# Kernel tuning notes

Measured on AMD Instinct MI355X. Metric: run time of the kernel, lower is better.

## Reference

```python
import jax, jax.numpy as jnp
import numpy as np

N_NODES = 100000
N_EDGES = 300000


def _nnconv(x, src, dst, edge_attr, w, b, root, bias, in_dim, out_dim):
    # PyG NNConv with aggr='add': W_e = nn(edge_attr_e).reshape(in, out)
    # msg_e = x[src_e] @ W_e ; out_i = sum_e->i msg_e + x_i @ root + bias
    W = (edge_attr @ w.T + b).reshape(-1, in_dim, out_dim)        # [E, in, out]
    msg = jnp.einsum('ei,eio->eo', x[src], W)                     # [E, out]
    agg = jax.ops.segment_sum(msg, dst, num_segments=x.shape[0])  # [N, out]
    return agg + x @ root + bias


def setup_inputs() -> dict:
    key = jax.random.key(0)
    ks = jax.random.split(key, 16)
    x = jax.random.normal(ks[0], (N_NODES, 2), dtype=jnp.float32)
    edge_index = jax.random.randint(ks[1], (2, N_EDGES), 0, N_NODES)
    edge_attr = jax.random.uniform(ks[2], (N_EDGES, 2), dtype=jnp.float32)

    def lin(k, out_d, in_d):
        s = 1.0 / np.sqrt(in_d)
        kw, kb = jax.random.split(k)
        w = jax.random.uniform(kw, (out_d, in_d), minval=-s, maxval=s)
        b = jax.random.uniform(kb, (out_d,), minval=-s, maxval=s)
        return w, b

    nn1_w, nn1_b = lin(ks[3], 64, 2)      # edge MLP for conv1: 2 -> 2*32
    nn2_w, nn2_b = lin(ks[4], 1024, 2)    # edge MLP for conv2: 2 -> 32*32
    root1 = jax.random.normal(ks[5], (2, 32)) * (1.0 / np.sqrt(2))
    bias1 = jnp.zeros((32,), dtype=jnp.float32)
    root2 = jax.random.normal(ks[6], (32, 32)) * (1.0 / np.sqrt(32))
    bias2 = jnp.zeros((32,), dtype=jnp.float32)
    fc1_w, fc1_b = lin(ks[7], 32, 32)
    fc2_w, fc2_b = lin(ks[8], 1, 32)
    return {
        'x': x, 'edge_index': edge_index, 'edge_attr': edge_attr,
        'nn1_w': nn1_w, 'nn1_b': nn1_b, 'root1': root1, 'bias1': bias1,
        'nn2_w': nn2_w, 'nn2_b': nn2_b, 'root2': root2, 'bias2': bias2,
        'fc1_w': fc1_w, 'fc1_b': fc1_b, 'fc2_w': fc2_w, 'fc2_b': fc2_b,
    }


def reference(x, edge_index, edge_attr, nn1_w, nn1_b, root1, bias1,
              nn2_w, nn2_b, root2, bias2, fc1_w, fc1_b, fc2_w, fc2_b):
    src, dst = edge_index[0], edge_index[1]
    h = jax.nn.relu(_nnconv(x, src, dst, edge_attr, nn1_w, nn1_b, root1, bias1, 2, 32))
    h = jax.nn.relu(_nnconv(h, src, dst, edge_attr, nn2_w, nn2_b, root2, bias2, 32, 32))
    h = jax.nn.relu(h @ fc1_w.T + fc1_b)
    return h @ fc2_w.T + fc2_b  # [N, 1]
```

## Files before the change

### kernel.cpp

```cpp
#include <hip/hip_runtime.h>

#define N_NODES 100000
#define N_EDGES 300000
#define CAP 32
#define NPAIRS (N_NODES / 2)
#define NT 64
#define NTILES ((N_NODES + NT - 1) / NT)
#define PAD 129

__global__ __launch_bounds__(256) void zero_cnt_kernel(int4* __restrict__ p,
                                                       int n4)
{
    int i = blockIdx.x * 256 + threadIdx.x;
    if (i < n4) p[i] = make_int4(0, 0, 0, 0);
}

__global__ __launch_bounds__(256) void scatter_kernel(
    const int* __restrict__ src, const int* __restrict__ dst,
    const float* __restrict__ ea,
    int* __restrict__ cnt, float4* __restrict__ slots)
{
    int e = blockIdx.x * 256 + threadIdx.x;
    if (e >= N_EDGES) return;
    int s = src[e], d = dst[e];
    float2 a = ((const float2*)ea)[e];
    int pos = atomicAdd(&cnt[d], 1);
    if (pos < CAP)
        slots[(size_t)d * CAP + pos] = make_float4(__int_as_float(s), a.x, a.y, 0.f);
}

__global__ __launch_bounds__(256) void prepack_kernel(
    const float* __restrict__ nn2_w, const float* __restrict__ nn2_b,
    const float* __restrict__ root2, const float* __restrict__ fc1_w,
    float* __restrict__ Wt, float* __restrict__ Ft)
{
    int t = blockIdx.x * 256 + threadIdx.x;
    if (t < 4096) {
        int i = t >> 5, o = t & 31;
        int ii = i & 31;
        float v;
        if (i < 32)      v = nn2_w[(ii * 32 + o) * 2];
        else if (i < 64) v = nn2_w[(ii * 32 + o) * 2 + 1];
        else if (i < 96) v = nn2_b[ii * 32 + o];
        else             v = root2[ii * 32 + o];
        Wt[i * 32 + o] = v;
    }
    if (t < 1024) {
        int o = t >> 5, j = t & 31;
        Ft[o * 32 + j] = fc1_w[j * 32 + o];
    }
}

__global__ __launch_bounds__(256) void layer1a_kernel(
    const float* __restrict__ x, const int* __restrict__ cnt,
    const float4* __restrict__ slots,
    const float* __restrict__ nn1_w, const float* __restrict__ nn1_b,
    const float* __restrict__ root1, const float* __restrict__ bias1,
    float* __restrict__ h1)
{
    int t = threadIdx.x;
    int wv = t >> 6, lane = t & 63, o = lane & 31, hihalf = lane >> 5;
    int pair = blockIdx.x * 4 + wv;
    if (pair >= NPAIRS) return;
    int n = pair * 2 + hihalf;
    int c = min(cnt[n], CAP);
    float u0 = 0.f, u1 = 0.f, u2 = 0.f, u3 = 0.f, u4 = 0.f, u5 = 0.f;
    if (o < c) {
        float4 sl = slots[(size_t)n * CAP + o];
        int s = __float_as_int(sl.x);
        float2 xv = ((const float2*)x)[s];
        u0 = xv.x * sl.y; u1 = xv.x * sl.z;
        u2 = xv.y * sl.y; u3 = xv.y * sl.z;
        u4 = xv.x;        u5 = xv.y;
    }
    #pragma unroll
    for (int m = 1; m < 32; m <<= 1) {
        u0 += __shfl_xor(u0, m, 32);
        u1 += __shfl_xor(u1, m, 32);
        u2 += __shfl_xor(u2, m, 32);
        u3 += __shfl_xor(u3, m, 32);
        u4 += __shfl_xor(u4, m, 32);
        u5 += __shfl_xor(u5, m, 32);
    }
    float2 w0 = ((const float2*)nn1_w)[o];
    float2 w1 = ((const float2*)nn1_w)[32 + o];
    float2 xn = ((const float2*)x)[n];
    float agg = u0 * w0.x + u1 * w0.y + u2 * w1.x + u3 * w1.y
              + u4 * nn1_b[o] + u5 * nn1_b[32 + o];
    float h = agg + fmaf(xn.x, root1[o], fmaf(xn.y, root1[32 + o], bias1[o]));
    h1[(size_t)n * 32 + o] = fmaxf(h, 0.f);
}

__global__ __launch_bounds__(256) void gather_uvw_kernel(
    const float* __restrict__ h1, const int* __restrict__ cnt,
    const float4* __restrict__ slots, float* __restrict__ UVW)
{
    int t = threadIdx.x, o = t & 31;
    int n = blockIdx.x * 8 + (t >> 5);
    if (n >= N_NODES) return;
    int c = min(cnt[n], CAP);
    float U = 0.f, V = 0.f, W = 0.f;
    for (int j0 = 0; j0 < c; j0 += 4) {
        bool g1 = j0 + 1 < c, g2 = j0 + 2 < c, g3 = j0 + 3 < c;
        float4 s0 = slots[(size_t)n * CAP + j0];
        float4 s1 = g1 ? slots[(size_t)n * CAP + j0 + 1] : s0;
        float4 s2 = g2 ? slots[(size_t)n * CAP + j0 + 2] : s0;
        float4 s3 = g3 ? slots[(size_t)n * CAP + j0 + 3] : s0;
        int i0 = __float_as_int(s0.x), i1 = __float_as_int(s1.x);
        int i2 = __float_as_int(s2.x), i3 = __float_as_int(s3.x);
        float v0 = h1[(size_t)i0 * 32 + o];
        float v1 = h1[(size_t)i1 * 32 + o];
        float v2 = h1[(size_t)i2 * 32 + o];
        float v3 = h1[(size_t)i3 * 32 + o];
        U = fmaf(s0.y, v0, U);
        U = fmaf(g1 ? s1.y : 0.f, v1, U);
        U = fmaf(g2 ? s2.y : 0.f, v2, U);
        U = fmaf(g3 ? s3.y : 0.f, v3, U);
        V = fmaf(s0.z, v0, V);
        V = fmaf(g1 ? s1.z : 0.f, v1, V);
        V = fmaf(g2 ? s2.z : 0.f, v2, V);
        V = fmaf(g3 ? s3.z : 0.f, v3, V);
        W += v0;
        W = fmaf(g1 ? 1.f : 0.f, v1, W);
        W = fmaf(g2 ? 1.f : 0.f, v2, W);
        W = fmaf(g3 ? 1.f : 0.f, v3, W);
    }
    size_t b = (size_t)n * 96;
    UVW[b + o]      = U;
    UVW[b + 32 + o] = V;
    UVW[b + 64 + o] = W;
}

__global__ __launch_bounds__(512, 6) void matvec_fc_kernel(
    const float* __restrict__ UVW, const float* __restrict__ h1,
    const float* __restrict__ Wt, const float* __restrict__ Ft,
    const float* __restrict__ bias2,
    const float* __restrict__ fc1_b, const float* __restrict__ fc2_w,
    const float* __restrict__ fc2_b, float* __restrict__ out)
{
    __shared__ float ld[NT][PAD];
    __shared__ float h2s[NT][33];
    float* psf = &ld[0][0];

    int t = threadIdx.x;
    int wv = t >> 6;
    int wvu = __builtin_amdgcn_readfirstlane(wv);
    int lane = t & 63;
    int tb = blockIdx.x * NT;

    {
        const float4* uvw4 = (const float4*)(UVW + (size_t)tb * 96);
        #pragma unroll
        for (int it = 0; it < 3; ++it) {
            int f4i = it * 512 + t;
            float4 v = uvw4[f4i];
            int node = f4i / 24, c4 = (f4i % 24) * 4;
            ld[node][c4]     = v.x;
            ld[node][c4 + 1] = v.y;
            ld[node][c4 + 2] = v.z;
            ld[node][c4 + 3] = v.w;
        }
        const float4* h14 = (const float4*)(h1 + (size_t)tb * 32);
        float4 v = h14[t];
        int node = t >> 3, c4 = 96 + (t & 7) * 4;
        ld[node][c4]     = v.x;
        ld[node][c4 + 1] = v.y;
        ld[node][c4 + 2] = v.z;
        ld[node][c4 + 3] = v.w;
    }
    __syncthreads();

    {
        int cb = 4 * wvu;
        float4 bb = *(const float4*)(bias2 + cb);
        float a0 = bb.x, a1 = bb.y, a2 = bb.z, a3 = bb.w;
        #pragma unroll 8
        for (int i = 0; i < 128; ++i) {
            float hv = ld[lane][i];
            float4 wA = *(const float4*)(Wt + i * 32 + cb);
            a0 = fmaf(hv, wA.x, a0); a1 = fmaf(hv, wA.y, a1);
            a2 = fmaf(hv, wA.z, a2); a3 = fmaf(hv, wA.w, a3);
        }
        h2s[lane][cb + 0] = fmaxf(a0, 0.f);
        h2s[lane][cb + 1] = fmaxf(a1, 0.f);
        h2s[lane][cb + 2] = fmaxf(a2, 0.f);
        h2s[lane][cb + 3] = fmaxf(a3, 0.f);
    }
    __syncthreads();

    {
        int cb = 4 * wvu;
        float4 fb = *(const float4*)(fc1_b + cb);
        float z0 = fb.x, z1 = fb.y, z2 = fb.z, z3 = fb.w;
        #pragma unroll 8
        for (int i = 0; i < 32; ++i) {
            float hv = h2s[lane][i];
            float4 fA = *(const float4*)(Ft + i * 32 + cb);
            z0 = fmaf(hv, fA.x, z0); z1 = fmaf(hv, fA.y, z1);
            z2 = fmaf(hv, fA.z, z2); z3 = fmaf(hv, fA.w, z3);
        }
        float4 cw = *(const float4*)(fc2_w + cb);
        float po = fmaxf(z0, 0.f) * cw.x + fmaxf(z1, 0.f) * cw.y
                 + fmaxf(z2, 0.f) * cw.z + fmaxf(z3, 0.f) * cw.w;
        __syncthreads();
        psf[wv * NT + lane] = po;
    }
    __syncthreads();
    if (wv == 0) {
        int n = tb + lane;
        if (n < N_NODES) {
            float s = psf[lane]          + psf[NT + lane]
                    + psf[2 * NT + lane] + psf[3 * NT + lane]
                    + psf[4 * NT + lane] + psf[5 * NT + lane]
                    + psf[6 * NT + lane] + psf[7 * NT + lane];
            out[n] = s + fc2_b[0];
        }
    }
}

extern "C" void kernel_launch(void* const* d_in, const int* in_sizes, int n_in,
                              void* d_out, int out_size, void* d_ws, size_t ws_size,
                              hipStream_t stream) {
    const float* x      = (const float*)d_in[0];
    const int*   ei     = (const int*)d_in[1];
    const float* ea     = (const float*)d_in[2];
    const float* nn1_w  = (const float*)d_in[3];
    const float* nn1_b  = (const float*)d_in[4];
    const float* root1  = (const float*)d_in[5];
    const float* bias1  = (const float*)d_in[6];
    const float* nn2_w  = (const float*)d_in[7];
    const float* nn2_b  = (const float*)d_in[8];
    const float* root2  = (const float*)d_in[9];
    const float* bias2  = (const float*)d_in[10];
    const float* fc1_w  = (const float*)d_in[11];
    const float* fc1_b  = (const float*)d_in[12];
    const float* fc2_w  = (const float*)d_in[13];
    const float* fc2_b  = (const float*)d_in[14];
    float* out = (float*)d_out;

    float* ws = (float*)d_ws;
    int*    cnt   = (int*)ws;
    float4* slots = (float4*)(ws + 262144);
    float*  h1    = ws + 262144 + (size_t)N_NODES * CAP * 4;
    float*  UVW   = h1 + (size_t)N_NODES * 32;
    float*  Wt    = UVW + (size_t)N_NODES * 96;
    float*  Ft    = Wt + 4096;

    const int* src = ei;
    const int* dst = ei + N_EDGES;

    zero_cnt_kernel<<<(N_NODES / 4 + 255) / 256, 256, 0, stream>>>(
        (int4*)cnt, N_NODES / 4);
    prepack_kernel<<<16, 256, 0, stream>>>(
        nn2_w, nn2_b, root2, fc1_w, Wt, Ft);
    scatter_kernel<<<(N_EDGES + 255) / 256, 256, 0, stream>>>(
        src, dst, ea, cnt, slots);
    layer1a_kernel<<<(NPAIRS + 3) / 4, 256, 0, stream>>>(
        x, cnt, slots, nn1_w, nn1_b, root1, bias1, h1);
    gather_uvw_kernel<<<(N_NODES + 7) / 8, 256, 0, stream>>>(
        h1, cnt, slots, UVW);
    matvec_fc_kernel<<<NTILES, 512, 0, stream>>>(
        UVW, h1, Wt, Ft, bias2, fc1_b, fc2_w, fc2_b, out);
}
```

Baseline: 94.61 us.

## Fold layer-1 edge aggregation into scatter via atomics and merge setup kernels

Layer-1 per-node sums (six scalars per node) are now accumulated in the scatter kernel with float atomicAdd instead of being gathered again from the slot lists. The h1 kernel then only reads these six sums per node. The zeroing and weight prepack kernels are merged into one setup kernel that also zeroes the new accumulator buffer. This saves a launch and the second pass over slots, but adds six float atomics per edge. It also makes the layer-1 summation order nondeterministic, and edges beyond CAP now count in layer 1 while the slot path still drops them.

Result: slower. 171.8 us (+81.5%).

```diff
diff --git a/kernel.cpp b/kernel.cpp
--- a/kernel.cpp
+++ b/kernel.cpp
@@ -3,22 +3,41 @@
 #define N_NODES 100000
 #define N_EDGES 300000
 #define CAP 32
-#define NPAIRS (N_NODES / 2)
 #define NT 64
 #define NTILES ((N_NODES + NT - 1) / NT)
 #define PAD 129
 
-__global__ __launch_bounds__(256) void zero_cnt_kernel(int4* __restrict__ p,
-                                                       int n4)
-{
-    int i = blockIdx.x * 256 + threadIdx.x;
-    if (i < n4) p[i] = make_int4(0, 0, 0, 0);
+__global__ __launch_bounds__(256) void setup_kernel(
+    int4* __restrict__ zbase,
+    const float* __restrict__ nn2_w, const float* __restrict__ nn2_b,
+    const float* __restrict__ root2, const float* __restrict__ fc1_w,
+    float* __restrict__ Wt, float* __restrict__ Ft)
+{
+    int gid = blockIdx.x * 256 + threadIdx.x;
+    int stride = gridDim.x * 256;
+    for (int i = gid; i < 175000; i += stride)
+        zbase[i] = make_int4(0, 0, 0, 0);
+    if (gid < 4096) {
+        int i = gid >> 5, o = gid & 31;
+        int ii = i & 31;
+        float v;
+        if (i < 32)      v = nn2_w[(ii * 32 + o) * 2];
+        else if (i < 64) v = nn2_w[(ii * 32 + o) * 2 + 1];
+        else if (i < 96) v = nn2_b[ii * 32 + o];
+        else             v = root2[ii * 32 + o];
+        Wt[i * 32 + o] = v;
+    }
+    if (gid < 1024) {
+        int o = gid >> 5, j = gid & 31;
+        Ft[o * 32 + j] = fc1_w[j * 32 + o];
+    }
 }
 
 __global__ __launch_bounds__(256) void scatter_kernel(
     const int* __restrict__ src, const int* __restrict__ dst,
-    const float* __restrict__ ea,
-    int* __restrict__ cnt, float4* __restrict__ slots)
+    const float* __restrict__ ea, const float* __restrict__ x,
+    int* __restrict__ cnt, float* __restrict__ u,
+    float4* __restrict__ slots)
 {
     int e = blockIdx.x * 256 + threadIdx.x;
     if (e >= N_EDGES) return;
@@ -27,67 +46,33 @@
     int pos = atomicAdd(&cnt[d], 1);
     if (pos < CAP)
         slots[(size_t)d * CAP + pos] = make_float4(__int_as_float(s), a.x, a.y, 0.f);
-}
-
-__global__ __launch_bounds__(256) void prepack_kernel(
-    const float* __restrict__ nn2_w, const float* __restrict__ nn2_b,
-    const float* __restrict__ root2, const float* __restrict__ fc1_w,
-    float* __restrict__ Wt, float* __restrict__ Ft)
-{
-    int t = blockIdx.x * 256 + threadIdx.x;
-    if (t < 4096) {
-        int i = t >> 5, o = t & 31;
-        int ii = i & 31;
-        float v;
-        if (i < 32)      v = nn2_w[(ii * 32 + o) * 2];
-        else if (i < 64) v = nn2_w[(ii * 32 + o) * 2 + 1];
-        else if (i < 96) v = nn2_b[ii * 32 + o];
-        else             v = root2[ii * 32 + o];
-        Wt[i * 32 + o] = v;
-    }
-    if (t < 1024) {
-        int o = t >> 5, j = t & 31;
-        Ft[o * 32 + j] = fc1_w[j * 32 + o];
-    }
-}
-
-__global__ __launch_bounds__(256) void layer1a_kernel(
-    const float* __restrict__ x, const int* __restrict__ cnt,
-    const float4* __restrict__ slots,
+    float2 xv = ((const float2*)x)[s];
+    atomicAdd(u + d,                xv.x * a.x);
+    atomicAdd(u + N_NODES + d,      xv.x * a.y);
+    atomicAdd(u + 2 * N_NODES + d,  xv.y * a.x);
+    atomicAdd(u + 3 * N_NODES + d,  xv.y * a.y);
+    atomicAdd(u + 4 * N_NODES + d,  xv.x);
+    atomicAdd(u + 5 * N_NODES + d,  xv.y);
+}
+
+__global__ __launch_bounds__(256) void h1_kernel(
+    const float* __restrict__ u, const float* __restrict__ x,
     const float* __restrict__ nn1_w, const float* __restrict__ nn1_b,
     const float* __restrict__ root1, const float* __restrict__ bias1,
     float* __restrict__ h1)
 {
-    int t = threadIdx.x;
-    int wv = t >> 6, lane = t & 63, o = lane & 31, hihalf = lane >> 5;
-    int pair = blockIdx.x * 4 + wv;
-    if (pair >= NPAIRS) return;
-    int n = pair * 2 + hihalf;
-    int c = min(cnt[n], CAP);
-    float u0 = 0.f, u1 = 0.f, u2 = 0.f, u3 = 0.f, u4 = 0.f, u5 = 0.f;
-    if (o < c) {
-        float4 sl = slots[(size_t)n * CAP + o];
-        int s = __float_as_int(sl.x);
-        float2 xv = ((const float2*)x)[s];
-        u0 = xv.x * sl.y; u1 = xv.x * sl.z;
-        u2 = xv.y * sl.y; u3 = xv.y * sl.z;
-        u4 = xv.x;        u5 = xv.y;
-    }
-    #pragma unroll
-    for (int m = 1; m < 32; m <<= 1) {
-        u0 += __shfl_xor(u0, m, 32);
-        u1 += __shfl_xor(u1, m, 32);
-        u2 += __shfl_xor(u2, m, 32);
-        u3 += __shfl_xor(u3, m, 32);
-        u4 += __shfl_xor(u4, m, 32);
-        u5 += __shfl_xor(u5, m, 32);
-    }
+    int t = threadIdx.x, o = t & 31;
+    int n = blockIdx.x * 8 + (t >> 5);
+    if (n >= N_NODES) return;
+    float u0 = u[n],               u1 = u[N_NODES + n];
+    float u2 = u[2 * N_NODES + n], u3 = u[3 * N_NODES + n];
+    float u4 = u[4 * N_NODES + n], u5 = u[5 * N_NODES + n];
     float2 w0 = ((const float2*)nn1_w)[o];
     float2 w1 = ((const float2*)nn1_w)[32 + o];
     float2 xn = ((const float2*)x)[n];
-    float agg = u0 * w0.x + u1 * w0.y + u2 * w1.x + u3 * w1.y
-              + u4 * nn1_b[o] + u5 * nn1_b[32 + o];
-    float h = agg + fmaf(xn.x, root1[o], fmaf(xn.y, root1[32 + o], bias1[o]));
+    float h = u0 * w0.x + u1 * w0.y + u2 * w1.x + u3 * w1.y
+            + u4 * nn1_b[o] + u5 * nn1_b[32 + o];
+    h += fmaf(xn.x, root1[o], fmaf(xn.y, root1[32 + o], bias1[o]));
     h1[(size_t)n * 32 + o] = fmaxf(h, 0.f);
 }
 
@@ -240,23 +225,22 @@
 
     float* ws = (float*)d_ws;
     int*    cnt   = (int*)ws;
-    float4* slots = (float4*)(ws + 262144);
-    float*  h1    = ws + 262144 + (size_t)N_NODES * CAP * 4;
-    float*  UVW   = h1 + (size_t)N_NODES * 32;
-    float*  Wt    = UVW + (size_t)N_NODES * 96;
+    float*  u     = ws + 100000;
+    float4* slots = (float4*)(ws + 700000);
+    float*  h1    = ws + 13500000;
+    float*  UVW   = ws + 16700000;
+    float*  Wt    = ws + 26300000;
     float*  Ft    = Wt + 4096;
 
     const int* src = ei;
     const int* dst = ei + N_EDGES;
 
-    zero_cnt_kernel<<<(N_NODES / 4 + 255) / 256, 256, 0, stream>>>(
-        (int4*)cnt, N_NODES / 4);
-    prepack_kernel<<<16, 256, 0, stream>>>(
-        nn2_w, nn2_b, root2, fc1_w, Wt, Ft);
+    setup_kernel<<<688, 256, 0, stream>>>(
+        (int4*)cnt, nn2_w, nn2_b, root2, fc1_w, Wt, Ft);
     scatter_kernel<<<(N_EDGES + 255) / 256, 256, 0, stream>>>(
-        src, dst, ea, cnt, slots);
-    layer1a_kernel<<<(NPAIRS + 3) / 4, 256, 0, stream>>>(
-        x, cnt, slots, nn1_w, nn1_b, root1, bias1, h1);
+        src, dst, ea, x, cnt, u, slots);
+    h1_kernel<<<(N_NODES + 7) / 8, 256, 0, stream>>>(
+        u, x, nn1_w, nn1_b, root1, bias1, h1);
     gather_uvw_kernel<<<(N_NODES + 7) / 8, 256, 0, stream>>>(
         h1, cnt, slots, UVW);
     matvec_fc_kernel<<<NTILES, 512, 0, stream>>>(
```

## Gather compact 8-float layer-1 sums and recompute h1 per edge in gather

Applied to the files above, without the earlier changes.

Layer 1 now writes only an 8-float per-node summary (edge-weighted sums plus own features) instead of a 32-wide h1 row. The gather kernel rebuilds h1 for each source neighbour on the fly from those 8 values and packed weights, then appends the node's own h1 as a fourth block, so the matvec kernel reads a single contiguous 128-wide row. The zero-fill and weight prepack kernels are merged into one setup kernel. This cuts random-gather traffic per edge from 128 to 32 bytes and drops a launch, at the cost of extra FMAs per edge and a larger UVWT buffer.

Result: slower. 103.9 us (+9.8%).

```diff
diff --git a/kernel.cpp b/kernel.cpp
--- a/kernel.cpp
+++ b/kernel.cpp
@@ -8,11 +8,45 @@
 #define NTILES ((N_NODES + NT - 1) / NT)
 #define PAD 129
 
-__global__ __launch_bounds__(256) void zero_cnt_kernel(int4* __restrict__ p,
-                                                       int n4)
-{
-    int i = blockIdx.x * 256 + threadIdx.x;
-    if (i < n4) p[i] = make_int4(0, 0, 0, 0);
+__global__ __launch_bounds__(256) void setup_kernel(
+    int4* __restrict__ zbase,
+    const float* __restrict__ nn2_w, const float* __restrict__ nn2_b,
+    const float* __restrict__ root2, const float* __restrict__ fc1_w,
+    const float* __restrict__ nn1_w, const float* __restrict__ nn1_b,
+    const float* __restrict__ root1,
+    float* __restrict__ Wt, float* __restrict__ Ft, float* __restrict__ W1t)
+{
+    int gid = blockIdx.x * 256 + threadIdx.x;
+    int stride = gridDim.x * 256;
+    for (int i = gid; i < 25000; i += stride)
+        zbase[i] = make_int4(0, 0, 0, 0);
+    if (gid < 4096) {
+        int i = gid >> 5, o = gid & 31;
+        int ii = i & 31;
+        float v;
+        if (i < 32)      v = nn2_w[(ii * 32 + o) * 2];
+        else if (i < 64) v = nn2_w[(ii * 32 + o) * 2 + 1];
+        else if (i < 96) v = nn2_b[ii * 32 + o];
+        else             v = root2[ii * 32 + o];
+        Wt[i * 32 + o] = v;
+    }
+    if (gid < 1024) {
+        int o = gid >> 5, j = gid & 31;
+        Ft[o * 32 + j] = fc1_w[j * 32 + o];
+    }
+    if (gid < 256) {
+        int k = gid >> 5, o = gid & 31;
+        float v;
+        if (k == 0)      v = nn1_w[2 * o];
+        else if (k == 1) v = nn1_w[2 * o + 1];
+        else if (k == 2) v = nn1_w[2 * (32 + o)];
+        else if (k == 3) v = nn1_w[2 * (32 + o) + 1];
+        else if (k == 4) v = nn1_b[o];
+        else if (k == 5) v = nn1_b[32 + o];
+        else if (k == 6) v = root1[o];
+        else             v = root1[32 + o];
+        W1t[k * 32 + o] = v;
+    }
 }
 
 __global__ __launch_bounds__(256) void scatter_kernel(
@@ -29,34 +63,9 @@
         slots[(size_t)d * CAP + pos] = make_float4(__int_as_float(s), a.x, a.y, 0.f);
 }
 
-__global__ __launch_bounds__(256) void prepack_kernel(
-    const float* __restrict__ nn2_w, const float* __restrict__ nn2_b,
-    const float* __restrict__ root2, const float* __restrict__ fc1_w,
-    float* __restrict__ Wt, float* __restrict__ Ft)
-{
-    int t = blockIdx.x * 256 + threadIdx.x;
-    if (t < 4096) {
-        int i = t >> 5, o = t & 31;
-        int ii = i & 31;
-        float v;
-        if (i < 32)      v = nn2_w[(ii * 32 + o) * 2];
-        else if (i < 64) v = nn2_w[(ii * 32 + o) * 2 + 1];
-        else if (i < 96) v = nn2_b[ii * 32 + o];
-        else             v = root2[ii * 32 + o];
-        Wt[i * 32 + o] = v;
-    }
-    if (t < 1024) {
-        int o = t >> 5, j = t & 31;
-        Ft[o * 32 + j] = fc1_w[j * 32 + o];
-    }
-}
-
-__global__ __launch_bounds__(256) void layer1a_kernel(
+__global__ __launch_bounds__(256) void u8_kernel(
     const float* __restrict__ x, const int* __restrict__ cnt,
-    const float4* __restrict__ slots,
-    const float* __restrict__ nn1_w, const float* __restrict__ nn1_b,
-    const float* __restrict__ root1, const float* __restrict__ bias1,
-    float* __restrict__ h1)
+    const float4* __restrict__ slots, float* __restrict__ u8)
 {
     int t = threadIdx.x;
     int wv = t >> 6, lane = t & 63, o = lane & 31, hihalf = lane >> 5;
@@ -82,22 +91,25 @@
         u4 += __shfl_xor(u4, m, 32);
         u5 += __shfl_xor(u5, m, 32);
     }
-    float2 w0 = ((const float2*)nn1_w)[o];
-    float2 w1 = ((const float2*)nn1_w)[32 + o];
     float2 xn = ((const float2*)x)[n];
-    float agg = u0 * w0.x + u1 * w0.y + u2 * w1.x + u3 * w1.y
-              + u4 * nn1_b[o] + u5 * nn1_b[32 + o];
-    float h = agg + fmaf(xn.x, root1[o], fmaf(xn.y, root1[32 + o], bias1[o]));
-    h1[(size_t)n * 32 + o] = fmaxf(h, 0.f);
-}
-
-__global__ __launch_bounds__(256) void gather_uvw_kernel(
-    const float* __restrict__ h1, const int* __restrict__ cnt,
-    const float4* __restrict__ slots, float* __restrict__ UVW)
+    float v = (o == 0) ? u0 : (o == 1) ? u1 : (o == 2) ? u2 : (o == 3) ? u3
+            : (o == 4) ? u4 : (o == 5) ? u5 : (o == 6) ? xn.x : xn.y;
+    if (o < 8) u8[(size_t)n * 8 + o] = v;
+}
+
+__global__ __launch_bounds__(256, 4) void gather_uvwt_kernel(
+    const float* __restrict__ u8, const int* __restrict__ cnt,
+    const float4* __restrict__ slots, const float* __restrict__ W1t,
+    const float* __restrict__ bias1, float* __restrict__ UVWT)
 {
     int t = threadIdx.x, o = t & 31;
     int n = blockIdx.x * 8 + (t >> 5);
-    if (n >= N_NODES) return;
+    float p0 = W1t[o],        p1 = W1t[32 + o],  p2 = W1t[64 + o];
+    float p3 = W1t[96 + o],   p4 = W1t[128 + o], p5 = W1t[160 + o];
+    float p6 = W1t[192 + o],  p7 = W1t[224 + o];
+    float bi = bias1[o];
+    const float4* u84 = (const float4*)u8;
+
     int c = min(cnt[n], CAP);
     float U = 0.f, V = 0.f, W = 0.f;
     for (int j0 = 0; j0 < c; j0 += 4) {
@@ -108,31 +120,58 @@
         float4 s3 = g3 ? slots[(size_t)n * CAP + j0 + 3] : s0;
         int i0 = __float_as_int(s0.x), i1 = __float_as_int(s1.x);
         int i2 = __float_as_int(s2.x), i3 = __float_as_int(s3.x);
-        float v0 = h1[(size_t)i0 * 32 + o];
-        float v1 = h1[(size_t)i1 * 32 + o];
-        float v2 = h1[(size_t)i2 * 32 + o];
-        float v3 = h1[(size_t)i3 * 32 + o];
-        U = fmaf(s0.y, v0, U);
-        U = fmaf(g1 ? s1.y : 0.f, v1, U);
-        U = fmaf(g2 ? s2.y : 0.f, v2, U);
-        U = fmaf(g3 ? s3.y : 0.f, v3, U);
-        V = fmaf(s0.z, v0, V);
-        V = fmaf(g1 ? s1.z : 0.f, v1, V);
-        V = fmaf(g2 ? s2.z : 0.f, v2, V);
-        V = fmaf(g3 ? s3.z : 0.f, v3, V);
-        W += v0;
-        W = fmaf(g1 ? 1.f : 0.f, v1, W);
-        W = fmaf(g2 ? 1.f : 0.f, v2, W);
-        W = fmaf(g3 ? 1.f : 0.f, v3, W);
-    }
-    size_t b = (size_t)n * 96;
-    UVW[b + o]      = U;
-    UVW[b + 32 + o] = V;
-    UVW[b + 64 + o] = W;
+        float4 a0 = u84[(size_t)i0 * 2],     b0 = u84[(size_t)i0 * 2 + 1];
+        float4 a1 = u84[(size_t)i1 * 2],     b1 = u84[(size_t)i1 * 2 + 1];
+        float4 a2 = u84[(size_t)i2 * 2],     b2 = u84[(size_t)i2 * 2 + 1];
+        float4 a3 = u84[(size_t)i3 * 2],     b3 = u84[(size_t)i3 * 2 + 1];
+        float h0 = bi, h1v = bi, h2v = bi, h3v = bi;
+        h0 = fmaf(a0.x, p0, h0); h0 = fmaf(a0.y, p1, h0);
+        h0 = fmaf(a0.z, p2, h0); h0 = fmaf(a0.w, p3, h0);
+        h0 = fmaf(b0.x, p4, h0); h0 = fmaf(b0.y, p5, h0);
+        h0 = fmaf(b0.z, p6, h0); h0 = fmaf(b0.w, p7, h0);
+        h1v = fmaf(a1.x, p0, h1v); h1v = fmaf(a1.y, p1, h1v);
+        h1v = fmaf(a1.z, p2, h1v); h1v = fmaf(a1.w, p3, h1v);
+        h1v = fmaf(b1.x, p4, h1v); h1v = fmaf(b1.y, p5, h1v);
+        h1v = fmaf(b1.z, p6, h1v); h1v = fmaf(b1.w, p7, h1v);
+        h2v = fmaf(a2.x, p0, h2v); h2v = fmaf(a2.y, p1, h2v);
+        h2v = fmaf(a2.z, p2, h2v); h2v = fmaf(a2.w, p3, h2v);
+        h2v = fmaf(b2.x, p4, h2v); h2v = fmaf(b2.y, p5, h2v);
+        h2v = fmaf(b2.z, p6, h2v); h2v = fmaf(b2.w, p7, h2v);
+        h3v = fmaf(a3.x, p0, h3v); h3v = fmaf(a3.y, p1, h3v);
+        h3v = fmaf(a3.z, p2, h3v); h3v = fmaf(a3.w, p3, h3v);
+        h3v = fmaf(b3.x, p4, h3v); h3v = fmaf(b3.y, p5, h3v);
+        h3v = fmaf(b3.z, p6, h3v); h3v = fmaf(b3.w, p7, h3v);
+        h0 = fmaxf(h0, 0.f);  h1v = fmaxf(h1v, 0.f);
+        h2v = fmaxf(h2v, 0.f); h3v = fmaxf(h3v, 0.f);
+        U = fmaf(s0.y, h0, U);
+        U = fmaf(g1 ? s1.y : 0.f, h1v, U);
+        U = fmaf(g2 ? s2.y : 0.f, h2v, U);
+        U = fmaf(g3 ? s3.y : 0.f, h3v, U);
+        V = fmaf(s0.z, h0, V);
+        V = fmaf(g1 ? s1.z : 0.f, h1v, V);
+        V = fmaf(g2 ? s2.z : 0.f, h2v, V);
+        V = fmaf(g3 ? s3.z : 0.f, h3v, V);
+        W += h0;
+        W = fmaf(g1 ? 1.f : 0.f, h1v, W);
+        W = fmaf(g2 ? 1.f : 0.f, h2v, W);
+        W = fmaf(g3 ? 1.f : 0.f, h3v, W);
+    }
+    float4 ta = u84[(size_t)n * 2], tb = u84[(size_t)n * 2 + 1];
+    float T = bi;
+    T = fmaf(ta.x, p0, T); T = fmaf(ta.y, p1, T);
+    T = fmaf(ta.z, p2, T); T = fmaf(ta.w, p3, T);
+    T = fmaf(tb.x, p4, T); T = fmaf(tb.y, p5, T);
+    T = fmaf(tb.z, p6, T); T = fmaf(tb.w, p7, T);
+    T = fmaxf(T, 0.f);
+    size_t b = (size_t)n * 128;
+    UVWT[b + o]      = U;
+    UVWT[b + 32 + o] = V;
+    UVWT[b + 64 + o] = W;
+    UVWT[b + 96 + o] = T;
 }
 
 __global__ __launch_bounds__(512, 6) void matvec_fc_kernel(
-    const float* __restrict__ UVW, const float* __restrict__ h1,
+    const float* __restrict__ UVWT,
     const float* __restrict__ Wt, const float* __restrict__ Ft,
     const float* __restrict__ bias2,
     const float* __restrict__ fc1_b, const float* __restrict__ fc2_w,
@@ -149,24 +188,17 @@
     int tb = blockIdx.x * NT;
 
     {
-        const float4* uvw4 = (const float4*)(UVW + (size_t)tb * 96);
+        const float4* uv4 = (const float4*)(UVWT + (size_t)tb * 128);
         #pragma unroll
-        for (int it = 0; it < 3; ++it) {
+        for (int it = 0; it < 4; ++it) {
             int f4i = it * 512 + t;
-            float4 v = uvw4[f4i];
-            int node = f4i / 24, c4 = (f4i % 24) * 4;
+            float4 v = uv4[f4i];
+            int node = f4i >> 5, c4 = (f4i & 31) * 4;
             ld[node][c4]     = v.x;
             ld[node][c4 + 1] = v.y;
             ld[node][c4 + 2] = v.z;
             ld[node][c4 + 3] = v.w;
         }
-        const float4* h14 = (const float4*)(h1 + (size_t)tb * 32);
-        float4 v = h14[t];
-        int node = t >> 3, c4 = 96 + (t & 7) * 4;
-        ld[node][c4]     = v.x;
-        ld[node][c4 + 1] = v.y;
-        ld[node][c4 + 2] = v.z;
-        ld[node][c4 + 3] = v.w;
     }
     __syncthreads();
 
@@ -240,25 +272,25 @@
 
     float* ws = (float*)d_ws;
     int*    cnt   = (int*)ws;
-    float4* slots = (float4*)(ws + 262144);
-    float*  h1    = ws + 262144 + (size_t)N_NODES * CAP * 4;
-    float*  UVW   = h1 + (size_t)N_NODES * 32;
-    float*  Wt    = UVW + (size_t)N_NODES * 96;
+    float*  u8    = ws + 100000;
+    float4* slots = (float4*)(ws + 900000);
+    float*  UVWT  = ws + 13700000;
+    float*  Wt    = ws + 26600000;
     float*  Ft    = Wt + 4096;
+    float*  W1t   = Ft + 1024;
 
     const int* src = ei;
     const int* dst = ei + N_EDGES;
 
-    zero_cnt_kernel<<<(N_NODES / 4 + 255) / 256, 256, 0, stream>>>(
-        (int4*)cnt, N_NODES / 4);
-    prepack_kernel<<<16, 256, 0, stream>>>(
-        nn2_w, nn2_b, root2, fc1_w, Wt, Ft);
+    setup_kernel<<<128, 256, 0, stream>>>(
+        (int4*)cnt, nn2_w, nn2_b, root2, fc1_w, nn1_w, nn1_b, root1,
+        Wt, Ft, W1t);
     scatter_kernel<<<(N_EDGES + 255) / 256, 256, 0, stream>>>(
         src, dst, ea, cnt, slots);
-    layer1a_kernel<<<(NPAIRS + 3) / 4, 256, 0, stream>>>(
-        x, cnt, slots, nn1_w, nn1_b, root1, bias1, h1);
-    gather_uvw_kernel<<<(N_NODES + 7) / 8, 256, 0, stream>>>(
-        h1, cnt, slots, UVW);
+    u8_kernel<<<(NPAIRS + 3) / 4, 256, 0, stream>>>(
+        x, cnt, slots, u8);
+    gather_uvwt_kernel<<<(N_NODES + 7) / 8, 256, 0, stream>>>(
+        u8, cnt, slots, W1t, bias1, UVWT);
     matvec_fc_kernel<<<NTILES, 512, 0, stream>>>(
-        UVW, h1, Wt, Ft, bias2, fc1_b, fc2_w, fc2_b, out);
-}
+        UVWT, Wt, Ft, bias2, fc1_b, fc2_w, fc2_b, out);
+}
```
